# Optimization experiments

Hardware: AMD Instinct MI355X
Metric: run time of the kernel (lower is better)

## Reference

```python
import jax, jax.numpy as jnp
import numpy as np

NC = 80
REG_MAX = 16
STRIDES = (8.0, 16.0, 32.0)
MAX_DET = 300
IOU_THR = 0.7
CONF_THR = 0.001
NCAND = 1024        # top candidates kept before greedy NMS
MAX_WH = 7680.0     # per-class offset trick (ultralytics max_wh)


def _make_anchors(shapes, strides, offset=0.5):
    pts, strs = [], []
    for (h, w), s in zip(shapes, strides):
        sx = jnp.arange(w, dtype=jnp.float32) + offset
        sy = jnp.arange(h, dtype=jnp.float32) + offset
        gy, gx = jnp.meshgrid(sy, sx, indexing='ij')
        pts.append(jnp.stack((gx, gy), -1).reshape(-1, 2))   # (h*w, 2)
        strs.append(jnp.full((h * w, 1), s, jnp.float32))
    return jnp.concatenate(pts, 0), jnp.concatenate(strs, 0)


def _decode_raw(feats):
    """feats_to_raw_yolov8: DFL decode + anchor transform -> pixel cxcywh + sigmoid cls."""
    B = feats[0].shape[0]
    no = 4 * REG_MAX + NC
    merged = jnp.concatenate([f.reshape(B, no, -1) for f in feats], axis=2)  # (B,no,A)
    dist, cls = merged[:, :4 * REG_MAX], merged[:, 4 * REG_MAX:]
    pd = dist.transpose(0, 2, 1).reshape(B, -1, 4, REG_MAX)                  # (B,A,4,reg_max)
    proj = jnp.arange(REG_MAX, dtype=merged.dtype)
    ltrb = jnp.einsum('bafr,r->baf', jax.nn.softmax(pd, -1), proj)           # (B,A,4)
    anchors, strd = _make_anchors([f.shape[2:] for f in feats], STRIDES)     # (A,2),(A,1)
    lt, rb = ltrb[..., :2], ltrb[..., 2:]
    x1y1 = anchors[None] - lt
    x2y2 = anchors[None] + rb
    cxy = (x1y1 + x2y2) * 0.5
    wh = x2y2 - x1y1
    dbox = jnp.concatenate((cxy, wh), -1) * strd[None]                       # (B,A,4) pixel cxcywh
    return dbox, jax.nn.sigmoid(cls).transpose(0, 2, 1)                      # (B,A,nc)


def _iou_one_vs_many(box, boxes):
    lt = jnp.maximum(box[:2], boxes[:, :2])
    rb = jnp.minimum(box[2:], boxes[:, 2:])
    inter = jnp.prod(jnp.clip(rb - lt, 0.0), -1)
    a1 = jnp.prod(box[2:] - box[:2])
    a2 = jnp.prod(boxes[:, 2:] - boxes[:, :2], -1)
    return inter / (a1 + a2 - inter + 1e-7)


def _nms_image(boxes_cxcywh, scores_cls):
    """conf threshold + per-class greedy NMS + max_det truncation -> (max_det, 6)."""
    conf = scores_cls.max(-1)                                   # (A,)
    cls = jnp.argmax(scores_cls, -1).astype(jnp.float32)        # (A,)
    conf = jnp.where(conf > CONF_THR, conf, 0.0)
    top_conf, idx = jax.lax.top_k(conf, NCAND)                  # candidate pre-selection
    cb = boxes_cxcywh[idx]                                      # (NCAND,4) cxcywh
    ccls = cls[idx]
    xy1 = cb[:, :2] - cb[:, 2:] * 0.5
    xy2 = cb[:, :2] + cb[:, 2:] * 0.5
    bx = jnp.concatenate((xy1, xy2), -1) + (ccls * MAX_WH)[:, None]  # class-offset xyxy

    def step(sc, _):
        j = jnp.argmax(sc)
        s = sc[j]
        sup = _iou_one_vs_many(bx[j], bx) > IOU_THR  # self-IoU=1 kills j as well
        return jnp.where(sup, 0.0, sc), (j, s)

    _, (sel, ss) = jax.lax.scan(step, top_conf, None, length=MAX_DET)
    rows = jnp.concatenate((cb[sel], ss[:, None], ccls[sel][:, None]), -1)  # (max_det,6)
    return jnp.where((ss > CONF_THR)[:, None], rows, 0.0)


def setup_inputs() -> dict:
    key = jax.random.key(0)
    k0, k1, k2 = jax.random.split(key, 3)
    B, no = 32, 4 * REG_MAX + NC
    return {
        'feat0': jax.random.normal(k0, (B, no, 80, 80), jnp.float32),
        'feat1': jax.random.normal(k1, (B, no, 40, 40), jnp.float32),
        'feat2': jax.random.normal(k2, (B, no, 20, 20), jnp.float32),
    }


def reference(feat0, feat1, feat2):
    dbox, ps = _decode_raw([feat0, feat1, feat2])        # (B,A,4), (B,A,nc)
    return jax.vmap(_nms_image)(dbox, ps)                # (B, max_det, 6)
```

## Files before the change

### kernel.cpp

```cpp
#include <hip/hip_runtime.h>
#include <stdint.h>

#define NCLS    80
#define NA_TOT  8400
#define NBATCH  32
#define MAXDET  300
#define SSORT   2048
#define RANKCAP 1536
#define CONFTHR 0.001f
#define TILES_PER_IMG 132
#define GKCAP   2056

__device__ __forceinline__ float xla_expf(float in) {
  const float exp_hi = 88.3762626647950f;
  const float exp_lo = -88.3762626647949f;
  const float LOG2EF = 1.44269504088896341f;
  const float C1 = 0.693359375f;
  const float C2 = -2.12194440e-4f;
  const float p0 = 1.9875691500E-4f, p1 = 1.3981999507E-3f, p2 = 8.3334519073E-3f;
  const float p3 = 4.1665795894E-2f, p4 = 1.6666665459E-1f, p5 = 5.0000001201E-1f;
  float x = fminf(fmaxf(in, exp_lo), exp_hi);
  float fx = floorf(__fadd_rn(__fmul_rn(x, LOG2EF), 0.5f));
  float tmp = __fmul_rn(C1, fx);
  float z   = __fmul_rn(C2, fx);
  x = __fsub_rn(x, tmp);
  x = __fsub_rn(x, z);
  float y = __fadd_rn(__fmul_rn(x, p0), p1);
  y = __fadd_rn(__fmul_rn(y, x), p2);
  y = __fadd_rn(__fmul_rn(y, x), p3);
  y = __fadd_rn(__fmul_rn(y, x), p4);
  y = __fadd_rn(__fmul_rn(y, x), p5);
  y = __fadd_rn(__fmul_rn(y, __fmul_rn(x, x)), x);
  y = __fadd_rn(1.0f, y);
  int m = (int)fx;
  float s = __uint_as_float((uint32_t)(m + 127) << 23);
  float r = __fmul_rn(y, s);
  return fmaxf(r, in);
}

__device__ __forceinline__ float xla_sigmoid(float v) {
  float e = xla_expf(-v);
  float den = __fadd_rn(1.0f, e);
  return 1.0f / den;
}

__device__ __forceinline__ void gload_lds16(const float* gp, float* lp) {
  __builtin_amdgcn_global_load_lds(
      (const __attribute__((address_space(1))) void*)gp,
      (__attribute__((address_space(3))) void*)lp, 16, 0, 0);
}

__global__ __launch_bounds__(256) void yolo_decode_kernel(
    const float* __restrict__ f0, const float* __restrict__ f1,
    const float* __restrict__ f2,
    float4* __restrict__ oboxes, float* __restrict__ oconf,
    float* __restrict__ oclsf) {
  __shared__ float sm[4 * 144 * 16];
  int bx  = blockIdx.x;
  int b   = bx / TILES_PER_IMG;
  int r   = bx - b * TILES_PER_IMG;
  int tid = threadIdx.x;
  int lane = tid & 63;
  int wv   = tid >> 6;

  const float* base; int Alvl, W, a0, lvlbase; float stridef;
  if (r < 100)      { base = f0 + (size_t)b * (144 * 6400); W = 80; Alvl = 6400;
                      a0 = r * 64; stridef = 8.0f; lvlbase = 0; }
  else if (r < 125) { base = f1 + (size_t)b * (144 * 1600); W = 40; Alvl = 1600;
                      a0 = (r - 100) * 64; stridef = 16.0f; lvlbase = 6400; }
  else              { base = f2 + (size_t)b * (144 * 400);  W = 20; Alvl = 400;
                      int aa = (r - 125) * 64; a0 = (aa + 64 <= 400) ? aa : 336;
                      stridef = 32.0f; lvlbase = 8000; }

  int a0w = a0 + wv * 16;
  float* Sw = sm + wv * (144 * 16);

  #pragma unroll
  for (int k = 0; k < 9; ++k) {
    int ch = k * 16 + (lane >> 2);
    const float* gp = base + (size_t)ch * Alvl + a0w + (lane & 3) * 4;
    gload_lds16(gp, Sw + k * 256);
  }
  asm volatile("s_waitcnt vmcnt(0)" ::: "memory");
  __builtin_amdgcn_sched_barrier(0);

  int idx = lane & 15;
  int w   = lane >> 4;
  int ai  = a0w + idx;
  float ax = __fadd_rn((float)(ai % W), 0.5f);
  float ay = __fadd_rn((float)(ai / W), 0.5f);

  float d[16];
  float mx = -INFINITY;
  #pragma unroll
  for (int rr = 0; rr < 16; ++rr) {
    d[rr] = Sw[(w * 16 + rr) * 16 + idx];
    mx = fmaxf(mx, d[rr]);
  }
  float e[16]; float ssum = 0.0f;
  #pragma unroll
  for (int rr = 0; rr < 16; ++rr) {
    e[rr] = xla_expf(__fsub_rn(d[rr], mx));
    ssum = __fadd_rn(ssum, e[rr]);
  }
  float acc = 0.0f;
  #pragma unroll
  for (int rr = 0; rr < 16; ++rr) {
    float p = e[rr] / ssum;
    acc = __fadd_rn(acc, __fmul_rn(p, (float)rr));
  }

  float lt0 = __shfl(acc, idx + 0);
  float lt1 = __shfl(acc, idx + 16);
  float lt2 = __shfl(acc, idx + 32);
  float lt3 = __shfl(acc, idx + 48);

  float best = -INFINITY, second = -INFINITY; int bi = 0;
  #pragma unroll 5
  for (int kk = 0; kk < 20; ++kk) {
    int c = 64 + w * 20 + kk;
    float v = Sw[c * 16 + idx];
    if (v > best)        { second = best; best = v; bi = w * 20 + kk; }
    else if (v > second) { second = v; }
  }
  float gb = __shfl(best, idx + 0), gs = __shfl(second, idx + 0);
  int   gi = __shfl(bi,   idx + 0);
  #pragma unroll
  for (int qq = 1; qq < 4; ++qq) {
    float bq = __shfl(best, idx + qq * 16), sq = __shfl(second, idx + qq * 16);
    int   iq = __shfl(bi,   idx + qq * 16);
    if (bq > gb) { gs = fmaxf(gb, sq); gb = bq; gi = iq; }
    else         { gs = fmaxf(gs, bq); }
  }

  float conf = 0.0f; int cls = gi;
  if (__fsub_rn(gb, gs) < 1e-4f || gb > 5.0f) {
    if (w == 0) {
      float bs = -INFINITY; int bj = 0;
      for (int kk = 0; kk < NCLS; ++kk) {
        float v = Sw[(64 + kk) * 16 + idx];
        float s2 = xla_sigmoid(v);
        if (s2 > bs) { bs = s2; bj = kk; }
      }
      conf = bs; cls = bj;
    }
  } else {
    conf = xla_sigmoid(gb);
  }

  if (w == 0) {
    float x1 = __fsub_rn(ax, lt0);
    float y1 = __fsub_rn(ay, lt1);
    float x2 = __fadd_rn(ax, lt2);
    float y2 = __fadd_rn(ay, lt3);
    float cx = __fmul_rn(__fadd_rn(x1, x2), 0.5f);
    float cy = __fmul_rn(__fadd_rn(y1, y2), 0.5f);
    float ww = __fsub_rn(x2, x1);
    float hh = __fsub_rn(y2, y1);
    int t = b * NA_TOT + lvlbase + a0w + idx;
    oboxes[t] = make_float4(__fmul_rn(cx, stridef), __fmul_rn(cy, stridef),
                            __fmul_rn(ww, stridef), __fmul_rn(hh, stridef));
    conf = (conf > CONFTHR) ? conf : 0.0f;
    oconf[t] = conf;
    oclsf[t] = (float)cls;
  }
}

struct __align__(16) K2Lds {
  unsigned confL[NA_TOT];
  unsigned hist[16][257];
  unsigned tot[257];
  unsigned Tarr[257];
};

__global__ __launch_bounds__(1024) void yolo_select_kernel(
    const float* __restrict__ conf,
    unsigned long long* __restrict__ g_keys, unsigned* __restrict__ g_scnt,
    float* __restrict__ g_rowd, unsigned long long* __restrict__ g_clsMask) {
  __shared__ K2Lds u;
  __shared__ unsigned s_need, s_prefix, s_found, s_B, s_scnt, s_cut, s_done;
  int b    = blockIdx.x;
  int tid  = threadIdx.x;
  int lane = tid & 63;
  int wv   = tid >> 6;
  const unsigned* confu = (const unsigned*)conf + (size_t)b * NA_TOT;
  unsigned long long* gk = g_keys + (size_t)b * GKCAP;

  for (int i = tid; i < NA_TOT; i += 1024) u.confL[i] = confu[i];
  {
    float4 z4 = make_float4(0.f, 0.f, 0.f, 0.f);
    float4* gr = (float4*)(g_rowd + (size_t)b * 1024 * 8);
    for (int k = tid; k < 2048; k += 1024) gr[k] = z4;
  }
  for (int i = tid; i < NCLS * 16; i += 1024)
    g_clsMask[(size_t)b * (NCLS * 16) + i] = 0ull;
  if (tid == 0) { s_need = 1024; s_prefix = 0; s_cut = 0; s_done = 0; s_scnt = 0; }
  __syncthreads();

  for (int lv = 0; lv < 4; ++lv) {
    __syncthreads();
    if (s_done) break;
    for (int i = tid; i < 16 * 257; i += 1024) ((unsigned*)u.hist)[i] = 0;
    if (tid == 0) { s_found = 0; s_B = 0; }
    __syncthreads();
    unsigned pfx = s_prefix;
    for (int it = 0; it < 9; ++it) {
      int i = tid + it * 1024;
      unsigned c = (i < NA_TOT) ? u.confL[i] : 0u;
      bool in; unsigned bin;
      if (lv == 0)      { in = true;                bin = c >> 23; }
      else if (lv == 1) { in = ((c >> 23) == pfx);  bin = (c >> 15) & 0xFF; }
      else if (lv == 2) { in = ((c >> 15) == pfx);  bin = (c >> 7) & 0xFF; }
      else              { in = ((c >> 7)  == pfx);  bin = c & 0x7F; }
      bool act = (c != 0) && in;
      unsigned long long ab = __ballot(act);
      if (ab) {
        int fl = __ffsll(ab) - 1;
        unsigned fbin = __shfl(bin, fl);
        unsigned long long same = __ballot(act && (bin == fbin));
        if (same == ab) {
          if (lane == fl) atomicAdd(&u.hist[wv][fbin], (unsigned)__popcll(ab));
        } else if (act) {
          atomicAdd(&u.hist[wv][bin], 1u);
        }
      }
    }
    __syncthreads();
    if (tid < 256) {
      unsigned s = 0;
      #pragma unroll
      for (int q = 0; q < 16; ++q) s += u.hist[q][tid];
      u.tot[tid] = s;
    }
    __syncthreads();
    if (tid < 64) {
      unsigned carry = 0;
      if (tid == 0) u.Tarr[256] = 0;
      for (int ch = 3; ch >= 0; --ch) {
        int bb = ch * 64 + tid;
        unsigned v = u.tot[bb];
        #pragma unroll
        for (int off = 1; off < 64; off <<= 1) {
          unsigned t2 = __shfl_down(v, off);
          if (tid + off < 64) v += t2;
        }
        u.Tarr[bb] = v + carry;
        carry += __shfl(v, 0);
      }
    }
    __syncthreads();
    unsigned need = s_need;
    if (tid < 256) {
      unsigned h = u.tot[tid];
      if (h > 0 && u.Tarr[tid + 1] < need && u.Tarr[tid + 1] + h >= need) {
        s_B = (unsigned)tid; s_found = 1;
      }
    }
    __syncthreads();
    if (tid == 0) {
      if (!s_found) { s_cut = 1; s_done = 1; }
      else {
        unsigned B = s_B;
        unsigned selcnt = (1024u - need) + u.Tarr[B];
        if (selcnt <= (unsigned)RANKCAP || lv == 3) {
          s_done = 1;
          if (lv == 0)      s_cut = B << 23;
          else if (lv == 1) s_cut = (s_prefix << 23) | (B << 15);
          else if (lv == 2) s_cut = (s_prefix << 15) | (B << 7);
          else              s_cut = (s_prefix << 7)  | B;
        } else {
          s_need   = need - u.Tarr[B + 1];
          s_prefix = (s_prefix << 8) | B;
        }
      }
    }
  }
  __syncthreads();

  unsigned cut = s_cut;
  for (int it = 0; it < 9; ++it) {
    int i = tid + it * 1024;
    unsigned c = (i < NA_TOT) ? u.confL[i] : 0u;
    bool sel = (c != 0 && c >= cut);
    unsigned long long bal = __ballot(sel);
    unsigned base2 = 0;
    if (lane == 0 && bal) base2 = atomicAdd(&s_scnt, (unsigned)__popcll(bal));
    base2 = __shfl(base2, 0);
    if (sel) {
      unsigned p = base2 + (unsigned)__popcll(bal & ((1ull << lane) - 1ull));
      if (p < SSORT)
        gk[p] = ((unsigned long long)c << 32) |
                (unsigned long long)(0xFFFFFFFFu - (unsigned)i);
    }
  }
  __syncthreads();
  if (tid == 0) {
    unsigned sc = s_scnt; if (sc > SSORT) sc = SSORT;
    g_scnt[b] = sc;
    if (sc & 1u) gk[sc] = 0ull;
  }
}

__global__ __launch_bounds__(256) void yolo_rank_kernel(
    const unsigned long long* __restrict__ g_keys,
    const unsigned* __restrict__ g_scnt,
    const float4* __restrict__ boxes, const float* __restrict__ clsf,
    float* __restrict__ g_rowd, unsigned long long* __restrict__ g_clsMask) {
  __shared__ __align__(16) unsigned long long lk[GKCAP];
  int bx   = blockIdx.x;
  int b    = bx >> 3;
  int part = bx & 7;
  int tid  = threadIdx.x;
  const unsigned long long* gk = g_keys + (size_t)b * GKCAP;
  unsigned scnt = g_scnt[b];
  unsigned snp  = (scnt + 1u) & ~1u;

  for (unsigned i = tid; i < snp; i += 256) lk[i] = gk[i];
  __syncthreads();

  unsigned e = (unsigned)(part * 256 + tid);
  if (e >= scnt) return;
  unsigned long long mykey = lk[e];
  unsigned r = 0;
  #pragma unroll 4
  for (unsigned j = 0; j < snp; j += 2) {
    ulonglong2 kk = *reinterpret_cast<const ulonglong2*>(&lk[j]);
    r += (kk.x > mykey) ? 1u : 0u;
    r += (kk.y > mykey) ? 1u : 0u;
  }

  if (r < 1024) {
    unsigned a = 0xFFFFFFFFu - (unsigned)(mykey & 0xFFFFFFFFull);
    float4 cb = boxes[(size_t)b * NA_TOT + a];
    float cls = clsf[(size_t)b * NA_TOT + a];
    float* rowd = g_rowd + (size_t)b * 1024 * 8;
    float4* gr = (float4*)(rowd + (size_t)r * 8);
    gr[0] = cb;
    gr[1] = make_float4(__uint_as_float((unsigned)(mykey >> 32)), cls, 0.f, 0.f);
    atomicOr(&g_clsMask[(size_t)b * (NCLS * 16) + (int)cls * 16 + (r >> 6)],
             1ull << (r & 63));
  }
}

struct K3Lds {
  unsigned long long rows[1024][16];
  float    rowdata[1024][6];
  unsigned long long am[16];
};

__global__ __launch_bounds__(1024) void yolo_nms_kernel(
    const float* __restrict__ g_rowd,
    const unsigned long long* __restrict__ g_clsMask,
    float* __restrict__ out) {
  __shared__ K3Lds u;
  __shared__ unsigned s_sticky, s_fill;
  int b    = blockIdx.x;
  int tid  = threadIdx.x;
  const unsigned long long* cm = g_clsMask + (size_t)b * (NCLS * 16);

  {
    const float4* gr = (const float4*)(g_rowd + ((size_t)b * 1024 + tid) * 8);
    float4 v0 = gr[0];
    float4 v1 = gr[1];
    u.rowdata[tid][0] = v0.x; u.rowdata[tid][1] = v0.y;
    u.rowdata[tid][2] = v0.z; u.rowdata[tid][3] = v0.w;
    u.rowdata[tid][4] = v1.x; u.rowdata[tid][5] = v1.y;
  }
  {
    unsigned long long* flat = &u.rows[0][0];
    for (int k = tid; k < 1024 * 16; k += 1024) flat[k] = 0ull;
  }
  if (tid < 16) u.am[tid] = 0ull;
  if (tid == 0) { s_sticky = 0xFFFFFFFFu; s_fill = 0; }
  __syncthreads();

  {
    float cls = u.rowdata[tid][5];
    int c = (int)cls;
    const unsigned long long* cmask = cm + c * 16;
    bool valid = (cmask[tid >> 6] >> (tid & 63)) & 1ull;
    if (valid) {
      float bx0 = u.rowdata[tid][0], by0 = u.rowdata[tid][1];
      float bw0 = u.rowdata[tid][2], bh0 = u.rowdata[tid][3];
      float off = __fmul_rn(cls, 7680.0f);
      float hw  = __fmul_rn(bw0, 0.5f), hh = __fmul_rn(bh0, 0.5f);
      float wx1 = __fadd_rn(__fsub_rn(bx0, hw), off);
      float wy1 = __fadd_rn(__fsub_rn(by0, hh), off);
      float wx2 = __fadd_rn(__fadd_rn(bx0, hw), off);
      float wy2 = __fadd_rn(__fadd_rn(by0, hh), off);
      float a1  = __fmul_rn(__fsub_rn(wx2, wx1), __fsub_rn(wy2, wy1));
      int sw = tid & 15;
      for (int q = 0; q < 16; ++q) {
        unsigned long long m = cmask[q];
        while (m) {
          int bit = __ffsll(m) - 1;
          m &= m - 1ull;
          int j = q * 64 + bit;
          float jx = u.rowdata[j][0], jy = u.rowdata[j][1];
          float jw = u.rowdata[j][2], jh = u.rowdata[j][3];
          float jhw = __fmul_rn(jw, 0.5f), jhh = __fmul_rn(jh, 0.5f);
          float jx1 = __fadd_rn(__fsub_rn(jx, jhw), off);
          float jy1 = __fadd_rn(__fsub_rn(jy, jhh), off);
          float jx2 = __fadd_rn(__fadd_rn(jx, jhw), off);
          float jy2 = __fadd_rn(__fadd_rn(jy, jhh), off);
          float ltx = fmaxf(wx1, jx1), lty = fmaxf(wy1, jy1);
          float rbx = fminf(wx2, jx2), rby = fminf(wy2, jy2);
          float iw = fmaxf(__fsub_rn(rbx, ltx), 0.0f);
          float ih = fmaxf(__fsub_rn(rby, lty), 0.0f);
          float inter = __fmul_rn(iw, ih);
          float a2 = __fmul_rn(__fsub_rn(jx2, jx1), __fsub_rn(jy2, jy1));
          float den = __fadd_rn(__fsub_rn(__fadd_rn(a1, a2), inter), 1e-7f);
          float iou = inter / den;
          if (iou > 0.7f)
            u.rows[tid][(j >> 6) ^ sw] |= (1ull << (j & 63));
        }
      }
    }
  }
  __syncthreads();

  if (tid < NCLS) {
    const unsigned long long* cmask = cm + tid * 16;
    unsigned long long alive[16];
    bool any = false;
    #pragma unroll
    for (int q = 0; q < 16; ++q) { alive[q] = cmask[q]; any |= (alive[q] != 0ull); }
    while (any) {
      int r = -1;
      #pragma unroll
      for (int q = 0; q < 16; ++q)
        if (r < 0 && alive[q]) r = q * 64 + (__ffsll(alive[q]) - 1);
      atomicOr(&u.am[r >> 6], 1ull << (r & 63));
      int sw = r & 15;
      unsigned long long selfw = u.rows[r][(r >> 6) ^ sw];
      bool selfbit = (selfw >> (r & 63)) & 1ull;
      if (!selfbit) { atomicMin(&s_sticky, (unsigned)r); break; }
      any = false;
      #pragma unroll
      for (int q = 0; q < 16; ++q) {
        alive[q] &= ~u.rows[r][q ^ sw];
        any |= (alive[q] != 0ull);
      }
    }
  }
  __syncthreads();

  unsigned rs = s_sticky;
  {
    unsigned r = (unsigned)tid;
    bool surv = (u.am[r >> 6] >> (r & 63)) & 1ull;
    if (surv && r <= rs) {
      unsigned e2 = 0;
      int hi = (int)(r >> 6);
      #pragma unroll
      for (int q = 0; q < 16; ++q) {
        unsigned long long m = u.am[q];
        if (q < hi)       e2 += (unsigned)__popcll(m);
        else if (q == hi) e2 += (unsigned)__popcll(m & ((1ull << (r & 63)) - 1ull));
      }
      if (e2 < MAXDET) {
        float* orow = out + (size_t)b * (MAXDET * 6) + (size_t)e2 * 6;
        orow[0] = u.rowdata[r][0];
        orow[1] = u.rowdata[r][1];
        orow[2] = u.rowdata[r][2];
        orow[3] = u.rowdata[r][3];
        orow[4] = u.rowdata[r][4];
        orow[5] = u.rowdata[r][5];
      }
    }
  }
  if (tid == 0) {
    unsigned fill;
    if (rs != 0xFFFFFFFFu) {
      unsigned es = 0;
      int hi = (int)(rs >> 6);
      #pragma unroll
      for (int q = 0; q < 16; ++q) {
        unsigned long long m = u.am[q];
        if (q < hi)       es += (unsigned)__popcll(m);
        else if (q == hi) es += (unsigned)__popcll(m & ((1ull << (rs & 63)) - 1ull));
      }
      fill = es + 1;
    } else {
      unsigned S = 0;
      #pragma unroll
      for (int q = 0; q < 16; ++q) S += (unsigned)__popcll(u.am[q]);
      fill = S;
    }
    s_fill = (fill > (unsigned)MAXDET) ? (unsigned)MAXDET : fill;
  }
  __syncthreads();

  {
    unsigned fill = s_fill;
    bool st = (rs != 0xFFFFFFFFu);
    float* orow = out + (size_t)b * (MAXDET * 6);
    for (int i = (int)fill * 6 + tid; i < MAXDET * 6; i += 1024) {
      float v = 0.0f;
      if (st) v = u.rowdata[rs][i - (i / 6) * 6];
      orow[i] = v;
    }
  }
}

extern "C" void kernel_launch(void* const* d_in, const int* in_sizes, int n_in,
                              void* d_out, int out_size, void* d_ws, size_t ws_size,
                              hipStream_t stream) {
  const float* f0 = (const float*)d_in[0];
  const float* f1 = (const float*)d_in[1];
  const float* f2 = (const float*)d_in[2];
  float* out = (float*)d_out;

  char* ws = (char*)d_ws;
  float4* boxes = (float4*)ws;
  float*  conf  = (float*)(ws + (size_t)NBATCH * NA_TOT * 16);
  float*  clsf  = (float*)(ws + (size_t)NBATCH * NA_TOT * 20);
  size_t off = (size_t)NBATCH * NA_TOT * 24;
  float*  rowd  = (float*)(ws + off);                         off += 1048576;
  unsigned long long* clsm  = (unsigned long long*)(ws + off); off += 327680;
  unsigned long long* gkeys = (unsigned long long*)(ws + off); off += (size_t)NBATCH * GKCAP * 8;
  unsigned* scnts = (unsigned*)(ws + off);

  yolo_decode_kernel<<<NBATCH * TILES_PER_IMG, 256, 0, stream>>>(
      f0, f1, f2, boxes, conf, clsf);
  yolo_select_kernel<<<NBATCH, 1024, 0, stream>>>(conf, gkeys, scnts,
                                                  rowd, clsm);
  yolo_rank_kernel<<<NBATCH * 8, 256, 0, stream>>>(gkeys, scnts, boxes, clsf,
                                                   rowd, clsm);
  yolo_nms_kernel<<<NBATCH, 1024, 0, stream>>>(rowd, clsm, out);
}
```

Baseline: 123.8 us.

## Split NMS into parallel suppression-row build kernel and walk kernel

New measurement: 130.5 us. +5.4%, slower.

```diff
diff --git a/kernel.cpp b/kernel.cpp
--- a/kernel.cpp
+++ b/kernel.cpp
@@ -342,81 +342,83 @@
   }
 }
 
-struct K3Lds {
-  unsigned long long rows[1024][16];
-  float    rowdata[1024][6];
-  unsigned long long am[16];
-};
-
-__global__ __launch_bounds__(1024) void yolo_nms_kernel(
+__global__ __launch_bounds__(256) void yolo_rowbuild_kernel(
     const float* __restrict__ g_rowd,
     const unsigned long long* __restrict__ g_clsMask,
+    unsigned long long* __restrict__ g_rows) {
+  int bx   = blockIdx.x;
+  int b    = bx >> 3;
+  int part = bx & 7;
+  int tid  = threadIdx.x;
+  int r    = part * 256 + tid;
+  const float* rowd = g_rowd + (size_t)b * 1024 * 8;
+  const float* rd = rowd + (size_t)r * 8;
+  float cls = rd[5];
+  int c = (int)cls;
+  const unsigned long long* cmask = g_clsMask + (size_t)b * (NCLS * 16) + c * 16;
+  bool valid = (cmask[r >> 6] >> (r & 63)) & 1ull;
+  if (!valid) return;
+
+  float bx0 = rd[0], by0 = rd[1], bw0 = rd[2], bh0 = rd[3];
+  float off = __fmul_rn(cls, 7680.0f);
+  float hw  = __fmul_rn(bw0, 0.5f), hh = __fmul_rn(bh0, 0.5f);
+  float wx1 = __fadd_rn(__fsub_rn(bx0, hw), off);
+  float wy1 = __fadd_rn(__fsub_rn(by0, hh), off);
+  float wx2 = __fadd_rn(__fadd_rn(bx0, hw), off);
+  float wy2 = __fadd_rn(__fadd_rn(by0, hh), off);
+  float a1  = __fmul_rn(__fsub_rn(wx2, wx1), __fsub_rn(wy2, wy1));
+
+  unsigned long long row[16];
+  #pragma unroll
+  for (int q = 0; q < 16; ++q) row[q] = 0ull;
+
+  for (int q = 0; q < 16; ++q) {
+    unsigned long long m = cmask[q];
+    while (m) {
+      int bit = __ffsll(m) - 1;
+      m &= m - 1ull;
+      int j = q * 64 + bit;
+      const float* jd = rowd + (size_t)j * 8;
+      float jx = jd[0], jy = jd[1], jw = jd[2], jh = jd[3];
+      float jhw = __fmul_rn(jw, 0.5f), jhh = __fmul_rn(jh, 0.5f);
+      float jx1 = __fadd_rn(__fsub_rn(jx, jhw), off);
+      float jy1 = __fadd_rn(__fsub_rn(jy, jhh), off);
+      float jx2 = __fadd_rn(__fadd_rn(jx, jhw), off);
+      float jy2 = __fadd_rn(__fadd_rn(jy, jhh), off);
+      float ltx = fmaxf(wx1, jx1), lty = fmaxf(wy1, jy1);
+      float rbx = fminf(wx2, jx2), rby = fminf(wy2, jy2);
+      float iw = fmaxf(__fsub_rn(rbx, ltx), 0.0f);
+      float ih = fmaxf(__fsub_rn(rby, lty), 0.0f);
+      float inter = __fmul_rn(iw, ih);
+      float a2 = __fmul_rn(__fsub_rn(jx2, jx1), __fsub_rn(jy2, jy1));
+      float den = __fadd_rn(__fsub_rn(__fadd_rn(a1, a2), inter), 1e-7f);
+      float iou = inter / den;
+      if (iou > 0.7f)
+        row[q] |= (1ull << (j & 63));
+    }
+  }
+
+  ulonglong2* gro = (ulonglong2*)(g_rows + ((size_t)b * 1024 + r) * 16);
+  #pragma unroll
+  for (int q = 0; q < 8; ++q)
+    gro[q] = make_ulonglong2(row[q * 2], row[q * 2 + 1]);
+}
+
+__global__ __launch_bounds__(1024) void yolo_walk_kernel(
+    const float* __restrict__ g_rowd,
+    const unsigned long long* __restrict__ g_clsMask,
+    const unsigned long long* __restrict__ g_rows,
     float* __restrict__ out) {
-  __shared__ K3Lds u;
+  __shared__ unsigned long long am[16];
   __shared__ unsigned s_sticky, s_fill;
-  int b    = blockIdx.x;
-  int tid  = threadIdx.x;
+  int b   = blockIdx.x;
+  int tid = threadIdx.x;
   const unsigned long long* cm = g_clsMask + (size_t)b * (NCLS * 16);
-
-  {
-    const float4* gr = (const float4*)(g_rowd + ((size_t)b * 1024 + tid) * 8);
-    float4 v0 = gr[0];
-    float4 v1 = gr[1];
-    u.rowdata[tid][0] = v0.x; u.rowdata[tid][1] = v0.y;
-    u.rowdata[tid][2] = v0.z; u.rowdata[tid][3] = v0.w;
-    u.rowdata[tid][4] = v1.x; u.rowdata[tid][5] = v1.y;
-  }
-  {
-    unsigned long long* flat = &u.rows[0][0];
-    for (int k = tid; k < 1024 * 16; k += 1024) flat[k] = 0ull;
-  }
-  if (tid < 16) u.am[tid] = 0ull;
+  const unsigned long long* gr = g_rows + (size_t)b * 1024 * 16;
+  const float* rowd = g_rowd + (size_t)b * 1024 * 8;
+
+  if (tid < 16) am[tid] = 0ull;
   if (tid == 0) { s_sticky = 0xFFFFFFFFu; s_fill = 0; }
-  __syncthreads();
-
-  {
-    float cls = u.rowdata[tid][5];
-    int c = (int)cls;
-    const unsigned long long* cmask = cm + c * 16;
-    bool valid = (cmask[tid >> 6] >> (tid & 63)) & 1ull;
-    if (valid) {
-      float bx0 = u.rowdata[tid][0], by0 = u.rowdata[tid][1];
-      float bw0 = u.rowdata[tid][2], bh0 = u.rowdata[tid][3];
-      float off = __fmul_rn(cls, 7680.0f);
-      float hw  = __fmul_rn(bw0, 0.5f), hh = __fmul_rn(bh0, 0.5f);
-      float wx1 = __fadd_rn(__fsub_rn(bx0, hw), off);
-      float wy1 = __fadd_rn(__fsub_rn(by0, hh), off);
-      float wx2 = __fadd_rn(__fadd_rn(bx0, hw), off);
-      float wy2 = __fadd_rn(__fadd_rn(by0, hh), off);
-      float a1  = __fmul_rn(__fsub_rn(wx2, wx1), __fsub_rn(wy2, wy1));
-      int sw = tid & 15;
-      for (int q = 0; q < 16; ++q) {
-        unsigned long long m = cmask[q];
-        while (m) {
-          int bit = __ffsll(m) - 1;
-          m &= m - 1ull;
-          int j = q * 64 + bit;
-          float jx = u.rowdata[j][0], jy = u.rowdata[j][1];
-          float jw = u.rowdata[j][2], jh = u.rowdata[j][3];
-          float jhw = __fmul_rn(jw, 0.5f), jhh = __fmul_rn(jh, 0.5f);
-          float jx1 = __fadd_rn(__fsub_rn(jx, jhw), off);
-          float jy1 = __fadd_rn(__fsub_rn(jy, jhh), off);
-          float jx2 = __fadd_rn(__fadd_rn(jx, jhw), off);
-          float jy2 = __fadd_rn(__fadd_rn(jy, jhh), off);
-          float ltx = fmaxf(wx1, jx1), lty = fmaxf(wy1, jy1);
-          float rbx = fminf(wx2, jx2), rby = fminf(wy2, jy2);
-          float iw = fmaxf(__fsub_rn(rbx, ltx), 0.0f);
-          float ih = fmaxf(__fsub_rn(rby, lty), 0.0f);
-          float inter = __fmul_rn(iw, ih);
-          float a2 = __fmul_rn(__fsub_rn(jx2, jx1), __fsub_rn(jy2, jy1));
-          float den = __fadd_rn(__fsub_rn(__fadd_rn(a1, a2), inter), 1e-7f);
-          float iou = inter / den;
-          if (iou > 0.7f)
-            u.rows[tid][(j >> 6) ^ sw] |= (1ull << (j & 63));
-        }
-      }
-    }
-  }
   __syncthreads();
 
   if (tid < NCLS) {
@@ -430,15 +432,15 @@
       #pragma unroll
       for (int q = 0; q < 16; ++q)
         if (r < 0 && alive[q]) r = q * 64 + (__ffsll(alive[q]) - 1);
-      atomicOr(&u.am[r >> 6], 1ull << (r & 63));
-      int sw = r & 15;
-      unsigned long long selfw = u.rows[r][(r >> 6) ^ sw];
+      atomicOr(&am[r >> 6], 1ull << (r & 63));
+      const unsigned long long* rw = gr + (size_t)r * 16;
+      unsigned long long selfw = rw[r >> 6];
       bool selfbit = (selfw >> (r & 63)) & 1ull;
       if (!selfbit) { atomicMin(&s_sticky, (unsigned)r); break; }
       any = false;
       #pragma unroll
       for (int q = 0; q < 16; ++q) {
-        alive[q] &= ~u.rows[r][q ^ sw];
+        alive[q] &= ~rw[q];
         any |= (alive[q] != 0ull);
       }
     }
@@ -448,24 +450,25 @@
   unsigned rs = s_sticky;
   {
     unsigned r = (unsigned)tid;
-    bool surv = (u.am[r >> 6] >> (r & 63)) & 1ull;
+    bool surv = (am[r >> 6] >> (r & 63)) & 1ull;
     if (surv && r <= rs) {
       unsigned e2 = 0;
       int hi = (int)(r >> 6);
       #pragma unroll
       for (int q = 0; q < 16; ++q) {
-        unsigned long long m = u.am[q];
+        unsigned long long m = am[q];
         if (q < hi)       e2 += (unsigned)__popcll(m);
         else if (q == hi) e2 += (unsigned)__popcll(m & ((1ull << (r & 63)) - 1ull));
       }
       if (e2 < MAXDET) {
+        const float* rd = rowd + (size_t)r * 8;
         float* orow = out + (size_t)b * (MAXDET * 6) + (size_t)e2 * 6;
-        orow[0] = u.rowdata[r][0];
-        orow[1] = u.rowdata[r][1];
-        orow[2] = u.rowdata[r][2];
-        orow[3] = u.rowdata[r][3];
-        orow[4] = u.rowdata[r][4];
-        orow[5] = u.rowdata[r][5];
+        orow[0] = rd[0];
+        orow[1] = rd[1];
+        orow[2] = rd[2];
+        orow[3] = rd[3];
+        orow[4] = rd[4];
+        orow[5] = rd[5];
       }
     }
   }
@@ -476,7 +479,7 @@
       int hi = (int)(rs >> 6);
       #pragma unroll
       for (int q = 0; q < 16; ++q) {
-        unsigned long long m = u.am[q];
+        unsigned long long m = am[q];
         if (q < hi)       es += (unsigned)__popcll(m);
         else if (q == hi) es += (unsigned)__popcll(m & ((1ull << (rs & 63)) - 1ull));
       }
@@ -484,7 +487,7 @@
     } else {
       unsigned S = 0;
       #pragma unroll
-      for (int q = 0; q < 16; ++q) S += (unsigned)__popcll(u.am[q]);
+      for (int q = 0; q < 16; ++q) S += (unsigned)__popcll(am[q]);
       fill = S;
     }
     s_fill = (fill > (unsigned)MAXDET) ? (unsigned)MAXDET : fill;
@@ -497,7 +500,7 @@
     float* orow = out + (size_t)b * (MAXDET * 6);
     for (int i = (int)fill * 6 + tid; i < MAXDET * 6; i += 1024) {
       float v = 0.0f;
-      if (st) v = u.rowdata[rs][i - (i / 6) * 6];
+      if (st) v = rowd[(size_t)rs * 8 + (i - (i / 6) * 6)];
       orow[i] = v;
     }
   }
@@ -519,7 +522,9 @@
   float*  rowd  = (float*)(ws + off);                         off += 1048576;
   unsigned long long* clsm  = (unsigned long long*)(ws + off); off += 327680;
   unsigned long long* gkeys = (unsigned long long*)(ws + off); off += (size_t)NBATCH * GKCAP * 8;
-  unsigned* scnts = (unsigned*)(ws + off);
+  unsigned* scnts = (unsigned*)(ws + off);                    off += 4096;
+  off = (off + 255) & ~(size_t)255;
+  unsigned long long* grows = (unsigned long long*)(ws + off);
 
   yolo_decode_kernel<<<NBATCH * TILES_PER_IMG, 256, 0, stream>>>(
       f0, f1, f2, boxes, conf, clsf);
@@ -527,5 +532,6 @@
                                                   rowd, clsm);
   yolo_rank_kernel<<<NBATCH * 8, 256, 0, stream>>>(gkeys, scnts, boxes, clsf,
                                                    rowd, clsm);
-  yolo_nms_kernel<<<NBATCH, 1024, 0, stream>>>(rowd, clsm, out);
-}
+  yolo_rowbuild_kernel<<<NBATCH * 8, 256, 0, stream>>>(rowd, clsm, grows);
+  yolo_walk_kernel<<<NBATCH, 1024, 0, stream>>>(rowd, clsm, grows, out);
+}
```
